# Kernel tuning notes

Measured on AMD Instinct MI355X. Metric: run time of the kernel, lower is better.

## Reference

```python
import jax, jax.numpy as jnp
import numpy as np

COST_CLASS, COST_BBOX, COST_GIOU = 2.0, 5.0, 2.0
ALPHA, GAMMA, EPS = 0.25, 2.0, 1e-8


def box_cxcywh_to_xyxy(x):
    cx, cy, w, h = x[..., 0], x[..., 1], x[..., 2], x[..., 3]
    return jnp.stack([cx - 0.5 * w, cy - 0.5 * h, cx + 0.5 * w, cy + 0.5 * h], axis=-1)


def generalized_box_iou(b1, b2):
    # b1: [N,4], b2: [M,4] in xyxy -> [N,M]
    a1 = (b1[:, 2] - b1[:, 0]) * (b1[:, 3] - b1[:, 1])
    a2 = (b2[:, 2] - b2[:, 0]) * (b2[:, 3] - b2[:, 1])
    lt = jnp.maximum(b1[:, None, :2], b2[None, :, :2])
    rb = jnp.minimum(b1[:, None, 2:], b2[None, :, 2:])
    wh = jnp.maximum(rb - lt, 0.0)
    inter = wh[..., 0] * wh[..., 1]
    union = a1[:, None] + a2[None, :] - inter
    iou = inter / jnp.maximum(union, 1e-6)
    elt = jnp.minimum(b1[:, None, :2], b2[None, :, :2])
    erb = jnp.maximum(b1[:, None, 2:], b2[None, :, 2:])
    ewh = jnp.maximum(erb - elt, 0.0)
    encl = ewh[..., 0] * ewh[..., 1]
    return iou - (encl - union) / jnp.maximum(encl, 1e-6)


def setup_inputs() -> dict:
    key = jax.random.key(0)
    k1, k2, k3, k4 = jax.random.split(key, 4)
    bs, nq, nc, nt = 16, 900, 80, 3200
    return {
        'pred_logits': jax.random.normal(k1, (bs, nq, nc), dtype=jnp.float32),
        'pred_boxes': jax.random.uniform(k2, (bs, nq, 4), dtype=jnp.float32),
        'tgt_labels': jax.random.randint(k3, (nt,), 0, nc, dtype=jnp.int32),
        'tgt_boxes': jax.random.uniform(k4, (nt, 4), dtype=jnp.float32),
    }


def reference(pred_logits, pred_boxes, tgt_labels, tgt_boxes):
    bs, nq, nc = pred_logits.shape
    out_prob = jax.nn.sigmoid(pred_logits.reshape(bs * nq, nc))  # [N, C]
    out_bbox = pred_boxes.reshape(bs * nq, 4)                    # [N, 4]

    p = out_prob[:, tgt_labels]  # [N, M] gather by target class
    neg_cost = (1.0 - ALPHA) * p ** GAMMA * (-jnp.log(1.0 - p + EPS))
    pos_cost = ALPHA * (1.0 - p) ** GAMMA * (-jnp.log(p + EPS))
    cost_class = pos_cost - neg_cost

    # L1 cdist: [N, M]
    cost_bbox = jnp.sum(jnp.abs(out_bbox[:, None, :] - tgt_boxes[None, :, :]), axis=-1)

    cost_giou = -generalized_box_iou(box_cxcywh_to_xyxy(out_bbox), box_cxcywh_to_xyxy(tgt_boxes))

    C = COST_BBOX * cost_bbox + COST_CLASS * cost_class + COST_GIOU * cost_giou
    C = jnp.nan_to_num(C, nan=1.0)
    return C.reshape(bs, nq, -1)
```

## Files before the change

kernel.cpp:

```cpp
#include <hip/hip_runtime.h>
#include <cmath>

#define NCC   80
#define QT    8
#define BLK   256
#define VT    4
#define NT_C  3200
#define NQB_C 14400
#define CPR   (NT_C / VT)
#define NRG   (NQB_C / QT)
#define CSTR  20

__global__ __launch_bounds__(BLK) void cost_fast(
    const float* __restrict__ logits,
    const float* __restrict__ pboxes,
    const int*   __restrict__ labels,
    const float* __restrict__ tboxes,
    float*       __restrict__ out)
{
    __shared__ float4 s_clsv[NCC * (CSTR / 4)];
    __shared__ float4 s_qraw[2 * QT];
    __shared__ float4 s_qxyxy[2 * QT];
    __shared__ float  s_qa[2 * QT];
    float* s_cls = (float*)s_clsv;

    const int w0  = blockIdx.x * BLK;
    const int rg0 = w0 / CPR;

    for (int t = threadIdx.x; t < NCC * 16; t += BLK) {
        const int lab = t >> 4;
        const int qi  = t & 15;
        const int rg  = min(rg0 + (qi >> 3), NRG - 1);
        const int row = rg * QT + (qi & 7);
        const float x   = logits[row * NCC + lab];
        const float p   = 1.0f / (1.0f + __expf(-x));
        const float om  = 1.0f - p;
        const float pos = 0.25f * om * om * (-__logf(p  + 1e-8f));
        const float neg = 0.75f * p  * p  * (-__logf(om + 1e-8f));
        s_cls[lab * CSTR + qi] = 2.0f * (pos - neg) + 2.0f;
    }
    if (threadIdx.x < 2 * QT) {
        const int g = threadIdx.x >> 3;
        const int rg = min(rg0 + g, NRG - 1);
        const float4 b = ((const float4*)pboxes)[rg * QT + (threadIdx.x & 7)];
        s_qraw[threadIdx.x]  = b;
        s_qxyxy[threadIdx.x] = make_float4(b.x - 0.5f * b.z, b.y - 0.5f * b.w,
                                           b.x + 0.5f * b.z, b.y + 0.5f * b.w);
        s_qa[threadIdx.x]    = b.z * b.w;
    }
    __syncthreads();

    const int w  = w0 + threadIdx.x;
    const int rg = w / CPR;
    const int c  = w - rg * CPR;
    const int j  = c * VT;
    const int g8 = (rg - rg0) * QT;
    const int g2 = (rg - rg0) * 2;

    const int4 lab4 = ((const int4*)labels)[c];
    const int labk[VT] = { lab4.x, lab4.y, lab4.z, lab4.w };
    float4 tb[VT];
    float tx0[VT], ty0[VT], tx1[VT], ty1[VT], ta[VT];
#pragma unroll
    for (int k = 0; k < VT; ++k) {
        tb[k]  = ((const float4*)tboxes)[j + k];
        tx0[k] = tb[k].x - 0.5f * tb[k].z;  tx1[k] = tb[k].x + 0.5f * tb[k].z;
        ty0[k] = tb[k].y - 0.5f * tb[k].w;  ty1[k] = tb[k].y + 0.5f * tb[k].w;
        ta[k]  = tb[k].z * tb[k].w;
    }
    float4 c2f[VT][2];
#pragma unroll
    for (int k = 0; k < VT; ++k) {
        const int rbase = labk[k] * (CSTR / 4) + g2;
        c2f[k][0] = s_clsv[rbase];
        c2f[k][1] = s_clsv[rbase + 1];
    }

    const size_t obase = (size_t)(rg * QT) * NT_C + j;
#pragma unroll
    for (int q = 0; q < QT; ++q) {
        const int    qi = g8 + q;
        const float4 qb = s_qraw[qi];
        const float4 qx = s_qxyxy[qi];
        const float  qa = s_qa[qi];
        float res[VT];
#pragma unroll
        for (int k = 0; k < VT; ++k) {
            const float c2 = ((q & 4) ? c2f[k][1] : c2f[k][0])[q & 3];
            const float l1 = (fabsf(qb.x - tb[k].x) + fabsf(qb.y - tb[k].y))
                           + (fabsf(qb.z - tb[k].z) + fabsf(qb.w - tb[k].w));
            const float ltx = fmaxf(qx.x, tx0[k]), lty = fmaxf(qx.y, ty0[k]);
            const float rbx = fminf(qx.z, tx1[k]), rby = fminf(qx.w, ty1[k]);
            const float iw  = fmaxf(rbx - ltx, 0.0f);
            const float ih  = fmaxf(rby - lty, 0.0f);
            const float inter = iw * ih;
            const float uni   = (qa + ta[k]) - inter;
            const float ew  = fmaxf(qx.z, tx1[k]) - fminf(qx.x, tx0[k]);
            const float eh  = fmaxf(qx.w, ty1[k]) - fminf(qx.y, ty0[k]);
            const float encl = ew * eh;
            const float r1 = __builtin_amdgcn_rcpf(fmaxf(uni,  1e-6f));
            const float r2 = __builtin_amdgcn_rcpf(fmaxf(encl, 1e-6f));
            float cc = fmaf(5.0f, l1, c2);
            cc = fmaf(-2.0f * inter, r1, cc);
            cc = fmaf(-2.0f * uni,  r2, cc);
            res[k] = cc;
        }
        *(float4*)(out + obase + (size_t)q * NT_C) =
            make_float4(res[0], res[1], res[2], res[3]);
    }
}

__global__ __launch_bounds__(BLK) void cost_generic(
    const float* __restrict__ logits, const float* __restrict__ pboxes,
    const int* __restrict__ labels, const float* __restrict__ tboxes,
    float* __restrict__ out, int NQB, int NT, int NC)
{
    extern __shared__ float smem[];
    float*  s_cls = smem;
    float4* s_qb  = (float4*)(smem + QT * NC);

    const int i0 = blockIdx.y * QT;
    const int j  = blockIdx.x * BLK + threadIdx.x;

    for (int t = threadIdx.x; t < QT * NC; t += BLK) {
        const int qi = i0 + t / NC;
        float v = 0.0f;
        if (qi < NQB) {
            const float x  = logits[qi * NC + (t % NC)];
            const float p  = 1.0f / (1.0f + __expf(-x));
            const float om = 1.0f - p;
            v = 0.25f * om * om * (-__logf(p + 1e-8f))
              - 0.75f * p * p * (-__logf(om + 1e-8f));
        }
        s_cls[t] = v;
    }
    if (threadIdx.x < QT) {
        const int qi = i0 + threadIdx.x;
        s_qb[threadIdx.x] = (qi < NQB) ? ((const float4*)pboxes)[qi]
                                       : make_float4(0.f, 0.f, 0.f, 0.f);
    }
    __syncthreads();
    if (j >= NT) return;

    const float4 tb = ((const float4*)tboxes)[j];
    const int   lab = labels[j];
    const float tx0 = tb.x - 0.5f * tb.z, tx1 = tb.x + 0.5f * tb.z;
    const float ty0 = tb.y - 0.5f * tb.w, ty1 = tb.y + 0.5f * tb.w;
    const float ta  = tb.z * tb.w;

#pragma unroll
    for (int q = 0; q < QT; ++q) {
        const float4 qb = s_qb[q];
        const float ccls = s_cls[q * NC + lab];
        const float l1 = fabsf(qb.x - tb.x) + fabsf(qb.y - tb.y)
                       + fabsf(qb.z - tb.z) + fabsf(qb.w - tb.w);
        const float qx0 = qb.x - 0.5f * qb.z, qx1 = qb.x + 0.5f * qb.z;
        const float qy0 = qb.y - 0.5f * qb.w, qy1 = qb.y + 0.5f * qb.w;
        const float qa  = qb.z * qb.w;
        const float ltx = fmaxf(qx0, tx0), lty = fmaxf(qy0, ty0);
        const float rbx = fminf(qx1, tx1), rby = fminf(qy1, ty1);
        const float iw = fmaxf(rbx - ltx, 0.f), ih = fmaxf(rby - lty, 0.f);
        const float inter = iw * ih;
        const float uni   = qa + ta - inter;
        const float iou   = inter * __builtin_amdgcn_rcpf(fmaxf(uni, 1e-6f));
        const float ex0 = fminf(qx0, tx0), ey0 = fminf(qy0, ty0);
        const float ex1 = fmaxf(qx1, tx1), ey1 = fmaxf(qy1, ty1);
        const float ew = fmaxf(ex1 - ex0, 0.f), eh = fmaxf(ey1 - ey0, 0.f);
        const float encl = ew * eh;
        const float giou = iou - (encl - uni) * __builtin_amdgcn_rcpf(fmaxf(encl, 1e-6f));
        float cc = 5.0f * l1 + 2.0f * ccls - 2.0f * giou;
        cc = (cc == cc) ? cc : 1.0f;
        const int qi = i0 + q;
        if (qi < NQB) out[(size_t)qi * NT + j] = cc;
    }
}

extern "C" void kernel_launch(void* const* d_in, const int* in_sizes, int n_in,
                              void* d_out, int out_size, void* d_ws, size_t ws_size,
                              hipStream_t stream) {
    const float* logits = (const float*)d_in[0];
    const float* pboxes = (const float*)d_in[1];
    const int*   labels = (const int*)d_in[2];
    const float* tboxes = (const float*)d_in[3];
    float*       out    = (float*)d_out;

    const int nqb = in_sizes[1] / 4;
    const int nt  = in_sizes[2];
    const int nc  = in_sizes[0] / nqb;

    if (nqb == NQB_C && nt == NT_C && nc == NCC) {
        const int nblk = (NRG * CPR) / BLK;
        hipLaunchKernelGGL(cost_fast, dim3(nblk), dim3(BLK), 0, stream,
                           logits, pboxes, labels, tboxes, out);
    } else {
        dim3 grid((nt + BLK - 1) / BLK, (nqb + QT - 1) / QT);
        size_t sm = QT * nc * sizeof(float) + QT * sizeof(float4);
        hipLaunchKernelGGL(cost_generic, grid, dim3(BLK), sm, stream,
                           logits, pboxes, labels, tboxes, out, nqb, nt, nc);
    }
}
```

Baseline: 61.83 us.

## Skip redundant class-cost rows, nontemporal stores, and split query loop into halves

The class-cost precompute now computes only one 8-query group when a block does not straddle two row groups, which roughly halves the transcendental work in most blocks. The output is written with nontemporal vector stores to avoid polluting the cache with the large streaming result. The query loop is split into two non-unrolled halves that load four class costs at a time, and the enclosing box width and height are derived algebraically from the intersection deltas. Together these cut register pressure and ALU work. The risk is 32-bit offset arithmetic and a possible loss of instruction-level parallelism from the non-unrolled outer loop.

```diff
diff --git a/kernel.cpp b/kernel.cpp
--- a/kernel.cpp
+++ b/kernel.cpp
@@ -11,6 +11,16 @@
 #define NRG   (NQB_C / QT)
 #define CSTR  20
 
+typedef float f32x4 __attribute__((ext_vector_type(4)));
+
+__device__ __forceinline__ float cls_cost(float x) {
+    const float p   = 1.0f / (1.0f + __expf(-x));
+    const float om  = 1.0f - p;
+    const float pos = 0.25f * om * om * (-__logf(p  + 1e-8f));
+    const float neg = 0.75f * p  * p  * (-__logf(om + 1e-8f));
+    return 2.0f * (pos - neg) + 2.0f;
+}
+
 __global__ __launch_bounds__(BLK) void cost_fast(
     const float* __restrict__ logits,
     const float* __restrict__ pboxes,
@@ -19,34 +29,36 @@
     float*       __restrict__ out)
 {
     __shared__ float4 s_clsv[NCC * (CSTR / 4)];
-    __shared__ float4 s_qraw[2 * QT];
-    __shared__ float4 s_qxyxy[2 * QT];
+    __shared__ float4 s_qb[2 * QT];
+    __shared__ float4 s_qx[2 * QT];
     __shared__ float  s_qa[2 * QT];
     float* s_cls = (float*)s_clsv;
 
-    const int w0  = blockIdx.x * BLK;
-    const int rg0 = w0 / CPR;
-
-    for (int t = threadIdx.x; t < NCC * 16; t += BLK) {
-        const int lab = t >> 4;
-        const int qi  = t & 15;
-        const int rg  = min(rg0 + (qi >> 3), NRG - 1);
-        const int row = rg * QT + (qi & 7);
-        const float x   = logits[row * NCC + lab];
-        const float p   = 1.0f / (1.0f + __expf(-x));
-        const float om  = 1.0f - p;
-        const float pos = 0.25f * om * om * (-__logf(p  + 1e-8f));
-        const float neg = 0.75f * p  * p  * (-__logf(om + 1e-8f));
-        s_cls[lab * CSTR + qi] = 2.0f * (pos - neg) + 2.0f;
-    }
-    if (threadIdx.x < 2 * QT) {
-        const int g = threadIdx.x >> 3;
-        const int rg = min(rg0 + g, NRG - 1);
+    const int  w0  = blockIdx.x * BLK;
+    const int  rg0 = w0 / CPR;
+    const bool two = (((w0 + BLK - 1) / CPR) != rg0);
+
+    if (two) {
+        for (int t = threadIdx.x; t < 2 * QT * NCC; t += BLK) {
+            const int lab = t >> 4, qi = t & 15;
+            const int row = (rg0 + (qi >> 3)) * QT + (qi & 7);
+            s_cls[lab * CSTR + qi] = cls_cost(logits[row * NCC + lab]);
+        }
+    } else {
+        for (int t = threadIdx.x; t < QT * NCC; t += BLK) {
+            const int lab = t >> 3, qi = t & 7;
+            const int row = rg0 * QT + qi;
+            s_cls[lab * CSTR + qi] = cls_cost(logits[row * NCC + lab]);
+        }
+    }
+    const int ng = two ? 2 * QT : QT;
+    if (threadIdx.x < ng) {
+        const int rg = rg0 + (threadIdx.x >> 3);
         const float4 b = ((const float4*)pboxes)[rg * QT + (threadIdx.x & 7)];
-        s_qraw[threadIdx.x]  = b;
-        s_qxyxy[threadIdx.x] = make_float4(b.x - 0.5f * b.z, b.y - 0.5f * b.w,
-                                           b.x + 0.5f * b.z, b.y + 0.5f * b.w);
-        s_qa[threadIdx.x]    = b.z * b.w;
+        s_qb[threadIdx.x] = b;
+        s_qx[threadIdx.x] = make_float4(b.x - 0.5f * b.z, b.y - 0.5f * b.w,
+                                        b.x + 0.5f * b.z, b.y + 0.5f * b.w);
+        s_qa[threadIdx.x] = b.z * b.w;
     }
     __syncthreads();
 
@@ -55,7 +67,6 @@
     const int c  = w - rg * CPR;
     const int j  = c * VT;
     const int g8 = (rg - rg0) * QT;
-    const int g2 = (rg - rg0) * 2;
 
     const int4 lab4 = ((const int4*)labels)[c];
     const int labk[VT] = { lab4.x, lab4.y, lab4.z, lab4.w };
@@ -68,45 +79,50 @@
         ty0[k] = tb[k].y - 0.5f * tb[k].w;  ty1[k] = tb[k].y + 0.5f * tb[k].w;
         ta[k]  = tb[k].z * tb[k].w;
     }
-    float4 c2f[VT][2];
-#pragma unroll
-    for (int k = 0; k < VT; ++k) {
-        const int rbase = labk[k] * (CSTR / 4) + g2;
-        c2f[k][0] = s_clsv[rbase];
-        c2f[k][1] = s_clsv[rbase + 1];
-    }
-
-    const size_t obase = (size_t)(rg * QT) * NT_C + j;
-#pragma unroll
-    for (int q = 0; q < QT; ++q) {
-        const int    qi = g8 + q;
-        const float4 qb = s_qraw[qi];
-        const float4 qx = s_qxyxy[qi];
-        const float  qa = s_qa[qi];
-        float res[VT];
-#pragma unroll
-        for (int k = 0; k < VT; ++k) {
-            const float c2 = ((q & 4) ? c2f[k][1] : c2f[k][0])[q & 3];
-            const float l1 = (fabsf(qb.x - tb[k].x) + fabsf(qb.y - tb[k].y))
-                           + (fabsf(qb.z - tb[k].z) + fabsf(qb.w - tb[k].w));
-            const float ltx = fmaxf(qx.x, tx0[k]), lty = fmaxf(qx.y, ty0[k]);
-            const float rbx = fminf(qx.z, tx1[k]), rby = fminf(qx.w, ty1[k]);
-            const float iw  = fmaxf(rbx - ltx, 0.0f);
-            const float ih  = fmaxf(rby - lty, 0.0f);
-            const float inter = iw * ih;
-            const float uni   = (qa + ta[k]) - inter;
-            const float ew  = fmaxf(qx.z, tx1[k]) - fminf(qx.x, tx0[k]);
-            const float eh  = fmaxf(qx.w, ty1[k]) - fminf(qx.y, ty0[k]);
-            const float encl = ew * eh;
-            const float r1 = __builtin_amdgcn_rcpf(fmaxf(uni,  1e-6f));
-            const float r2 = __builtin_amdgcn_rcpf(fmaxf(encl, 1e-6f));
-            float cc = fmaf(5.0f, l1, c2);
-            cc = fmaf(-2.0f * inter, r1, cc);
-            cc = fmaf(-2.0f * uni,  r2, cc);
-            res[k] = cc;
-        }
-        *(float4*)(out + obase + (size_t)q * NT_C) =
-            make_float4(res[0], res[1], res[2], res[3]);
+
+    const unsigned obase = (unsigned)(rg * QT) * NT_C + (unsigned)j;
+
+#pragma unroll 1
+    for (int h = 0; h < 2; ++h) {
+        const int qbase = g8 + h * 4;
+        float4 c2v[VT];
+#pragma unroll
+        for (int k = 0; k < VT; ++k)
+            c2v[k] = *(const float4*)&s_cls[labk[k] * CSTR + qbase];
+
+        const unsigned offh = obase + (unsigned)h * 4u * NT_C;
+#pragma unroll
+        for (int q4 = 0; q4 < 4; ++q4) {
+            const int    qi = qbase + q4;
+            const float4 qb = s_qb[qi];
+            const float4 qx = s_qx[qi];
+            const float  qa = s_qa[qi];
+            float res[VT];
+#pragma unroll
+            for (int k = 0; k < VT; ++k) {
+                const float c2 = c2v[k][q4];
+                const float dx = fminf(qx.z, tx1[k]) - fmaxf(qx.x, tx0[k]);
+                const float dy = fminf(qx.w, ty1[k]) - fmaxf(qx.y, ty0[k]);
+                const float iw = fmaxf(dx, 0.0f);
+                const float ih = fmaxf(dy, 0.0f);
+                const float inter = iw * ih;
+                const float uni   = (qa + ta[k]) - inter;
+                const float ew = (qb.z + tb[k].z) - dx;
+                const float eh = (qb.w + tb[k].w) - dy;
+                const float encl = ew * eh;
+                const float r1 = __builtin_amdgcn_rcpf(fmaxf(uni,  1e-6f));
+                const float r2 = __builtin_amdgcn_rcpf(fmaxf(encl, 1e-6f));
+                const float l1 = (fabsf(qb.x - tb[k].x) + fabsf(qb.y - tb[k].y))
+                               + (fabsf(qb.z - tb[k].z) + fabsf(qb.w - tb[k].w));
+                float cc = fmaf(5.0f, l1, c2);
+                cc = fmaf(-2.0f * inter, r1, cc);
+                cc = fmaf(-2.0f * uni,  r2, cc);
+                res[k] = cc;
+            }
+            f32x4 v = { res[0], res[1], res[2], res[3] };
+            __builtin_nontemporal_store(
+                v, (f32x4*)(out + offh + (unsigned)q4 * NT_C));
+        }
     }
 }
 
```

Measured after the change: 56.11 us. -9.3%, faster.
